# Kernel optimization log

Hardware: AMD Instinct MI355X
Metric: run time of the kernel (lower is better)

The kernel has to match this reference:

```python
import jax, jax.numpy as jnp
import numpy as np

N_USER, N_ITEM = 60000, 60000
N = N_USER + N_ITEM
E_BASE = 1500000
P = 200000
IN_DIM, HID, OUT = 128, 128, 64
K_MAX = 0.5


def setup_inputs() -> dict:
    key = jax.random.key(0)
    ks = jax.random.split(key, 20)
    feat_user = jax.random.normal(ks[0], (N_USER, 256), jnp.float32)
    feat_item = jax.random.normal(ks[1], (N_ITEM, 128), jnp.float32)
    src_b = jax.random.randint(ks[2], (E_BASE,), 0, N, jnp.int32)
    dst_b = jax.random.randint(ks[3], (E_BASE,), 0, N, jnp.int32)
    loops = jnp.arange(N, dtype=jnp.int32)  # dgl.add_self_loop
    src = jnp.concatenate([src_b, loops])
    dst = jnp.concatenate([dst_b, loops])
    pos_src = jax.random.randint(ks[4], (P,), 0, N, jnp.int32)
    pos_dst = jax.random.randint(ks[5], (P,), 0, N, jnp.int32)
    neg_src = jax.random.randint(ks[6], (P,), 0, N, jnp.int32)
    neg_dst = jax.random.randint(ks[7], (P,), 0, N, jnp.int32)
    s = 0.05
    W_user = jax.random.normal(ks[8], (256, IN_DIM), jnp.float32) * s
    b_user = jnp.zeros((IN_DIM,), jnp.float32)
    W_item = jax.random.normal(ks[9], (128, IN_DIM), jnp.float32) * s
    b_item = jnp.zeros((IN_DIM,), jnp.float32)
    W_gat = jax.random.normal(ks[10], (IN_DIM, HID), jnp.float32) * s
    attn_l = jax.random.normal(ks[11], (HID,), jnp.float32) * s
    attn_r = jax.random.normal(ks[12], (HID,), jnp.float32) * s
    gat_bias = jnp.zeros((HID,), jnp.float32)
    W_pred = jax.random.normal(ks[13], (HID, OUT), jnp.float32) * s
    b_pred = jnp.zeros((OUT,), jnp.float32)
    return {
        "feat_user": feat_user, "feat_item": feat_item,
        "W_user": W_user, "b_user": b_user, "W_item": W_item, "b_item": b_item,
        "W_gat": W_gat, "attn_l": attn_l, "attn_r": attn_r, "gat_bias": gat_bias,
        "W_pred": W_pred, "b_pred": b_pred,
        "src": src, "dst": dst,
        "pos_src": pos_src, "pos_dst": pos_dst,
        "neg_src": neg_src, "neg_dst": neg_dst,
        "alpha_T": 1,
    }


def _gat_conv(x, src, dst, W_gat, attn_l, attn_r, gat_bias):
    # DGL GATConv, 1 head: fc (no bias), additive attention, edge softmax over dst.
    z = x @ W_gat                              # [N, HID]
    el = z @ attn_l                            # [N]
    er = z @ attn_r                            # [N]
    e = jax.nn.leaky_relu(el[src] + er[dst], 0.2)   # [E]
    m = jax.ops.segment_max(e, dst, num_segments=N)  # per-dst max (self loops -> no empty segs)
    ex = jnp.exp(e - m[dst])
    ssum = jax.ops.segment_sum(ex, dst, num_segments=N)
    a = ex / ssum[dst]                          # edge softmax coeffs
    msg = z[src] * a[:, None]                   # [E, HID]
    out = jax.ops.segment_sum(msg, dst, num_segments=N) + gat_bias
    return jax.nn.elu(out)                      # activation=F.elu


def _hold_loss(score, k_T):
    l = jax.nn.log_sigmoid(score)
    hold = k_T * jnp.max(l)
    l = jnp.where(l > hold, 0.0, l)
    return -jnp.sum(l)


def reference(feat_user, feat_item, W_user, b_user, W_item, b_item,
              W_gat, attn_l, attn_r, gat_bias, W_pred, b_pred,
              src, dst, pos_src, pos_dst, neg_src, neg_dst, alpha_T):
    # per-type input projection then concat in ntype order (dgl.to_homogeneous)
    hu = feat_user @ W_user + b_user
    hi = feat_item @ W_item + b_item
    x = jnp.concatenate([hu, hi], axis=0)       # [N, IN_DIM]
    h = _gat_conv(x, src, dst, W_gat, attn_l, attn_r, gat_bias)
    pos_score = jnp.sum(h[pos_src] * h[pos_dst], axis=1)
    neg_score = jnp.sum(h[neg_src] * h[neg_dst], axis=1)
    k_T = K_MAX if K_MAX <= alpha_T else alpha_T   # k_T = min(k_max, alpha_T)
    loss = _hold_loss(pos_score, k_T) + _hold_loss(neg_score, k_T)
    out = h[:N_USER] @ W_pred + b_pred          # predict_type 'user' == type id 0
    return loss, out
```

## Files before the change

### kernel.cpp

```cpp
#include <hip/hip_runtime.h>
#include <hip/hip_bf16.h>
#include <math.h>

#define NUSER 60000
#define NITEM 60000
#define NNODE 120000
#define BSH 9
#define NB 235
#define CAP 8192

typedef __attribute__((ext_vector_type(8))) short bf16x8;
typedef __attribute__((ext_vector_type(4))) float f32x4;
typedef __attribute__((ext_vector_type(2))) float f32x2;
typedef __attribute__((ext_vector_type(4))) unsigned short u16x4;

__device__ __forceinline__ float leaky02(float x) { return x > 0.f ? x : 0.2f * x; }

__device__ __forceinline__ float inv_ord(unsigned int u) {
  unsigned int bits = (u & 0x80000000u) ? (u & 0x7FFFFFFFu) : ~u;
  return __uint_as_float(bits);
}
__device__ __forceinline__ unsigned int ord_of(float f) {
  unsigned int u = __float_as_uint(f);
  return (u & 0x80000000u) ? ~u : (u | 0x80000000u);
}
__device__ __forceinline__ short f2bs(float f) {
  __hip_bfloat16 h = __float2bfloat16(f);
  return *reinterpret_cast<short*>(&h);
}

__device__ __forceinline__ void f8fma(f32x2& acc, float w, unsigned int u) {
  f32x2 zz = __builtin_amdgcn_cvt_pk_f32_fp8(u, false);
  f32x2 ww; ww.x = w; ww.y = w;
  acc = __builtin_elementwise_fma(ww, zz, acc);
}
__device__ __forceinline__ void fp8dot(f32x2& acc, unsigned int ua, unsigned int ub) {
  f32x2 a0 = __builtin_amdgcn_cvt_pk_f32_fp8(ua, false);
  f32x2 a1 = __builtin_amdgcn_cvt_pk_f32_fp8(ua, true);
  f32x2 b0 = __builtin_amdgcn_cvt_pk_f32_fp8(ub, false);
  f32x2 b1 = __builtin_amdgcn_cvt_pk_f32_fp8(ub, true);
  acc = __builtin_elementwise_fma(a0, b0, acc);
  acc = __builtin_elementwise_fma(a1, b1, acc);
}

__global__ __launch_bounds__(256) void prep_kernel(
    const float* __restrict__ Wu, const float* __restrict__ bu, const float* __restrict__ Wi,
    const float* __restrict__ bi, const float* __restrict__ Wg, const float* __restrict__ Wp,
    __hip_bfloat16* __restrict__ Bp_u, __hip_bfloat16* __restrict__ Bp_i,
    __hip_bfloat16* __restrict__ Bp_p, float* __restrict__ bf_u, float* __restrict__ bf_i) {
  int t = blockIdx.x * 256 + threadIdx.x;
  if (t < 32768) {
    int j = t & 7, lane = (t >> 3) & 63, rest = t >> 9;
    int nt = rest & 7, ks = rest >> 3;
    int k = ks * 32 + ((lane >> 4) << 3) + j;
    int n = nt * 16 + (lane & 15);
    float acc = 0.f;
#pragma unroll 8
    for (int jj = 0; jj < 128; ++jj) acc = fmaf(Wu[k * 128 + jj], Wg[jj * 128 + n], acc);
    Bp_u[t] = __float2bfloat16(acc);
  } else if (t < 49152) {
    int tt = t - 32768;
    int j = tt & 7, lane = (tt >> 3) & 63, rest = tt >> 9;
    int nt = rest & 7, ks = rest >> 3;
    int k = ks * 32 + ((lane >> 4) << 3) + j;
    int n = nt * 16 + (lane & 15);
    float acc = 0.f;
#pragma unroll 8
    for (int jj = 0; jj < 128; ++jj) acc = fmaf(Wi[k * 128 + jj], Wg[jj * 128 + n], acc);
    Bp_i[tt] = __float2bfloat16(acc);
  } else if (t < 57344) {
    int tt = t - 49152;
    int j = tt & 7, lane = (tt >> 3) & 63, rest = tt >> 9;
    int nt = rest & 3, ks = rest >> 2;
    int k = ks * 32 + ((lane >> 4) << 3) + j;
    int n = nt * 16 + (lane & 15);
    Bp_p[tt] = __float2bfloat16(Wp[k * 64 + n]);
  } else if (t < 57344 + 256) {
    int n = t - 57344;
    if (n < 128) {
      float acc = 0.f;
      for (int jj = 0; jj < 128; ++jj) acc = fmaf(bu[jj], Wg[jj * 128 + n], acc);
      bf_u[n] = acc;
    } else {
      int nn = n - 128;
      float acc = 0.f;
      for (int jj = 0; jj < 128; ++jj) acc = fmaf(bi[jj], Wg[jj * 128 + nn], acc);
      bf_i[nn] = acc;
    }
  }
}

template <int K>
__device__ __forceinline__ void zgemm_body(
    char* smem, const float* __restrict__ A, const __hip_bfloat16* __restrict__ Bp,
    const float* __restrict__ bias, const float* __restrict__ al, const float* __restrict__ ar,
    unsigned char* __restrict__ z8, float* __restrict__ el, float* __restrict__ er, int M,
    int blk) {
  float(*lds)[140] = (float(*)[140])smem;
  const int lane = threadIdx.x & 63, wv = threadIdx.x >> 6;
  const int t = threadIdx.x;
  const int C4 = K / 4;
  for (int f = t; f < 64 * C4; f += 256) {
    int row = f / C4, c4 = f - row * C4;
    int grow = blk * 64 + row;
    if (grow >= M) grow = M - 1;
    float4 a = *(const float4*)(A + (size_t)grow * K + c4 * 4);
    u16x4 pk;
    pk[0] = (unsigned short)f2bs(a.x);
    pk[1] = (unsigned short)f2bs(a.y);
    pk[2] = (unsigned short)f2bs(a.z);
    pk[3] = (unsigned short)f2bs(a.w);
    unsigned int byte = (unsigned int)row * (K * 2) + (unsigned int)c4 * 8;
    byte ^= (row & 7) << 4;
    *(u16x4*)(smem + byte) = pk;
  }
  __syncthreads();
  const bf16x8* bp = (const bf16x8*)Bp;
  const int frow = wv * 16 + (lane & 15);
  f32x4 acc[8] = {};
#pragma unroll
  for (int ks = 0; ks < K / 32; ++ks) {
    unsigned int byte = (unsigned int)frow * (K * 2) + (unsigned int)(ks * 32 + ((lane >> 4) << 3)) * 2;
    byte ^= (frow & 7) << 4;
    bf16x8 af = *(const bf16x8*)(smem + byte);
#pragma unroll
    for (int nt = 0; nt < 8; ++nt) {
      bf16x8 bfr = bp[(ks * 8 + nt) * 64 + lane];
      acc[nt] = __builtin_amdgcn_mfma_f32_16x16x32_bf16(af, bfr, acc[nt], 0, 0, 0);
    }
  }
  __syncthreads();
#pragma unroll
  for (int nt = 0; nt < 8; ++nt) {
    float b = bias[nt * 16 + (lane & 15)];
#pragma unroll
    for (int r = 0; r < 4; ++r)
      lds[wv * 16 + (lane >> 4) * 4 + r][nt * 16 + (lane & 15)] = acc[nt][r] + b;
  }
  __syncthreads();
  int row = threadIdx.x >> 2;
  int q = threadIdx.x & 3;
  int gm = blk * 64 + row;
  float pl = 0.f, pr = 0.f;
  if (gm < M) {
    const float* lrow = &lds[row][q * 32];
#pragma unroll
    for (int v4 = 0; v4 < 4; ++v4) {
      float f[8];
#pragma unroll
      for (int j = 0; j < 8; ++j) {
        f[j] = lrow[v4 * 8 + j];
        int c = q * 32 + v4 * 8 + j;
        pl = fmaf(f[j], al[c], pl);
        pr = fmaf(f[j], ar[c], pr);
      }
      unsigned int w0 = (unsigned int)__builtin_amdgcn_cvt_pk_fp8_f32(f[0], f[1], 0, false);
      w0 = (unsigned int)__builtin_amdgcn_cvt_pk_fp8_f32(f[2], f[3], (int)w0, true);
      unsigned int w1 = (unsigned int)__builtin_amdgcn_cvt_pk_fp8_f32(f[4], f[5], 0, false);
      w1 = (unsigned int)__builtin_amdgcn_cvt_pk_fp8_f32(f[6], f[7], (int)w1, true);
      uint2 st; st.x = w0; st.y = w1;
      *(uint2*)(z8 + (size_t)gm * 128 + q * 32 + v4 * 8) = st;
    }
  }
  pl += __shfl_xor(pl, 1, 64); pl += __shfl_xor(pl, 2, 64);
  pr += __shfl_xor(pr, 1, 64); pr += __shfl_xor(pr, 2, 64);
  if (q == 0 && gm < M) { el[gm] = pl; er[gm] = pr; }
}

__global__ __launch_bounds__(256) void zgemm_kernel(
    const float* __restrict__ Au, const __hip_bfloat16* __restrict__ Bpu,
    const float* __restrict__ bfu, const float* __restrict__ Ai,
    const __hip_bfloat16* __restrict__ Bpi, const float* __restrict__ bfi,
    const float* __restrict__ al, const float* __restrict__ ar, unsigned char* __restrict__ z8,
    float* __restrict__ el, float* __restrict__ er, int GU) {
  __shared__ __align__(16) char smem[64 * 140 * 4];
  if ((int)blockIdx.x < GU)
    zgemm_body<256>(smem, Au, Bpu, bfu, al, ar, z8, el, er, NUSER, blockIdx.x);
  else
    zgemm_body<128>(smem, Ai, Bpi, bfi, al, ar, z8 + (size_t)NUSER * 128, el + NUSER, er + NUSER,
                    NITEM, blockIdx.x - GU);
}

__global__ __launch_bounds__(256) void predgemm_kernel(
    const __hip_bfloat16* __restrict__ h, const __hip_bfloat16* __restrict__ Bp,
    const float* __restrict__ bias, float* __restrict__ out, int M) {
  const int lane = threadIdx.x & 63, wv = threadIdx.x >> 6;
  const int m0 = blockIdx.x * 64 + wv * 16;
  int arow = m0 + (lane & 15);
  if (arow >= M) arow = M - 1;
  const bf16x8* a0 = (const bf16x8*)(h + (size_t)arow * 128) + (lane >> 4);
  const bf16x8* bp = (const bf16x8*)Bp;
  f32x4 acc[4] = {};
#pragma unroll
  for (int ks = 0; ks < 4; ++ks) {
    bf16x8 af = a0[ks * 4];
#pragma unroll
    for (int nt = 0; nt < 4; ++nt) {
      bf16x8 bfr = bp[(ks * 4 + nt) * 64 + lane];
      acc[nt] = __builtin_amdgcn_mfma_f32_16x16x32_bf16(af, bfr, acc[nt], 0, 0, 0);
    }
  }
#pragma unroll
  for (int nt = 0; nt < 4; ++nt) {
    int col = nt * 16 + (lane & 15);
    float b = bias[col];
#pragma unroll
    for (int r = 0; r < 4; ++r) {
      int m = m0 + (lane >> 4) * 4 + r;
      if (m < M) out[(size_t)m * 64 + col] = acc[nt][r] + b;
    }
  }
}

__global__ __launch_bounds__(256) void bcount_kernel(const int* __restrict__ dst,
                                                     int* __restrict__ btotal, int E) {
  __shared__ int cnt[NB];
  for (int t = threadIdx.x; t < NB; t += 256) cnt[t] = 0;
  __syncthreads();
  for (int i = blockIdx.x * 256 + threadIdx.x; i < E; i += gridDim.x * 256)
    atomicAdd(&cnt[dst[i] >> BSH], 1);
  __syncthreads();
  for (int t = threadIdx.x; t < NB; t += 256)
    if (cnt[t]) atomicAdd(&btotal[t], cnt[t]);
}

__global__ void bscan_kernel(const int* __restrict__ btotal, int* __restrict__ bstart,
                             int* __restrict__ gcur) {
  __shared__ int s[256];
  int t = threadIdx.x;
  int v = (t < NB) ? btotal[t] : 0;
  s[t] = v;
  __syncthreads();
  for (int off = 1; off < 256; off <<= 1) {
    int a = (t >= off) ? s[t - off] : 0;
    __syncthreads();
    s[t] += a;
    __syncthreads();
  }
  int excl = s[t] - v;
  if (t < NB) { bstart[t] = excl; gcur[t] = excl; }
  if (t == NB - 1) bstart[NB] = s[t];
}

__global__ __launch_bounds__(256) void bscatter_kernel(const int* __restrict__ src,
                                                       const int* __restrict__ dst,
                                                       int* __restrict__ gcur,
                                                       unsigned int* __restrict__ scratch, int E) {
  __shared__ int cnt[NB];
  __shared__ int base[NB];
  for (int t = threadIdx.x; t < NB; t += 256) cnt[t] = 0;
  __syncthreads();
  const int i0 = blockIdx.x * 4096;
  unsigned int v_[16];
  int b_[16], r_[16];
#pragma unroll
  for (int j = 0; j < 16; ++j) {
    int i = i0 + j * 256 + threadIdx.x;
    b_[j] = -1;
    if (i < E) {
      int d = dst[i];
      int s = src[i];
      int b = d >> BSH;
      b_[j] = b;
      r_[j] = atomicAdd(&cnt[b], 1);
      v_[j] = (unsigned int)s | ((unsigned int)(d & 511) << 17);
    }
  }
  __syncthreads();
  for (int t = threadIdx.x; t < NB; t += 256)
    base[t] = cnt[t] ? atomicAdd(&gcur[t], cnt[t]) : 0;
  __syncthreads();
#pragma unroll
  for (int j = 0; j < 16; ++j)
    if (b_[j] >= 0) scratch[base[b_[j]] + r_[j]] = v_[j];
}

__global__ __launch_bounds__(512) void bsort_kernel(const unsigned int* __restrict__ scratch,
                                                    const int* __restrict__ bstart,
                                                    int* __restrict__ offs, int* __restrict__ ssrc) {
  __shared__ unsigned int buf[CAP];
  __shared__ int cnt[512], scn[512], cur[512];
  int b = blockIdx.x, t = threadIdx.x;
  int s = bstart[b], e = bstart[b + 1], n = e - s;
  int d0 = b << BSH;
  int ndst = NNODE - d0;
  if (ndst > 512) ndst = 512;
  cnt[t] = 0;
  cur[t] = 0;
  __syncthreads();
  bool fit = (n <= CAP);
  if (fit) {
    for (int i = t; i < n; i += 512) {
      unsigned int v = scratch[s + i];
      buf[i] = v;
      atomicAdd(&cnt[v >> 17], 1);
    }
  } else {
    for (int i = t; i < n; i += 512) atomicAdd(&cnt[scratch[s + i] >> 17], 1);
  }
  __syncthreads();
  scn[t] = cnt[t];
  __syncthreads();
  for (int off = 1; off < 512; off <<= 1) {
    int a = (t >= off) ? scn[t - off] : 0;
    __syncthreads();
    scn[t] += a;
    __syncthreads();
  }
  int start = scn[t] - cnt[t];
  if (t < ndst) offs[d0 + t] = s + start;
  if (b == NB - 1 && t == 0) offs[NNODE] = e;
  __syncthreads();
  cnt[t] = start;
  __syncthreads();
  if (fit) {
    for (int i = t; i < n; i += 512) {
      unsigned int v = buf[i];
      int dl = v >> 17;
      int r = atomicAdd(&cur[dl], 1);
      ssrc[s + cnt[dl] + r] = (int)(v & 0x1FFFFu);
    }
  } else {
    for (int i = t; i < n; i += 512) {
      unsigned int v = scratch[s + i];
      int dl = v >> 17;
      int r = atomicAdd(&cur[dl], 1);
      ssrc[s + cnt[dl] + r] = (int)(v & 0x1FFFFu);
    }
  }
}

__global__ __launch_bounds__(256) void aggregate_kernel(
    const unsigned char* __restrict__ z8, const float* __restrict__ el,
    const float* __restrict__ er, const int* __restrict__ offs, const int* __restrict__ ssrc,
    const float* __restrict__ gat_bias, __hip_bfloat16* __restrict__ h,
    unsigned char* __restrict__ h8) {
  __shared__ __align__(16) float2 ew[4][128];
  int wv = threadIdx.x >> 6, lane = threadIdx.x & 63;
  int d = blockIdx.x * 4 + wv;
  int s0 = offs[d], s1 = offs[d + 1];
  int deg = s1 - s0;
  float erd = er[d];
  const unsigned short* zw = (const unsigned short*)z8;
  f32x2 acc = {0.f, 0.f};
  float ssum = 0.f;
  if (deg <= 128) {
    float w0 = 0.f, w1 = 0.f;
    int o0 = 0, o1 = 0;
    if (lane < deg) { int s = ssrc[s0 + lane]; o0 = s << 6; w0 = __expf(leaky02(el[s] + erd)); }
    if (64 + lane < deg) { int s = ssrc[s0 + 64 + lane]; o1 = s << 6; w1 = __expf(leaky02(el[s] + erd)); }
    ew[wv][lane] = make_float2(w0, __int_as_float(o0));
    ew[wv][64 + lane] = make_float2(w1, __int_as_float(o1));
    __builtin_amdgcn_wave_barrier();
    int i = 0;
    for (; i + 8 <= deg; i += 8) {
      float4 p0 = *(const float4*)&ew[wv][i];
      float4 p1 = *(const float4*)&ew[wv][i + 2];
      float4 p2 = *(const float4*)&ew[wv][i + 4];
      float4 p3 = *(const float4*)&ew[wv][i + 6];
      unsigned int u0 = zw[__float_as_uint(p0.y) + lane];
      unsigned int u1 = zw[__float_as_uint(p0.w) + lane];
      unsigned int u2 = zw[__float_as_uint(p1.y) + lane];
      unsigned int u3 = zw[__float_as_uint(p1.w) + lane];
      unsigned int u4 = zw[__float_as_uint(p2.y) + lane];
      unsigned int u5 = zw[__float_as_uint(p2.w) + lane];
      unsigned int u6 = zw[__float_as_uint(p3.y) + lane];
      unsigned int u7 = zw[__float_as_uint(p3.w) + lane];
      ssum += ((p0.x + p0.z) + (p1.x + p1.z)) + ((p2.x + p2.z) + (p3.x + p3.z));
      f8fma(acc, p0.x, u0); f8fma(acc, p0.z, u1);
      f8fma(acc, p1.x, u2); f8fma(acc, p1.z, u3);
      f8fma(acc, p2.x, u4); f8fma(acc, p2.z, u5);
      f8fma(acc, p3.x, u6); f8fma(acc, p3.z, u7);
    }
    for (; i + 2 <= deg; i += 2) {
      float4 p = *(const float4*)&ew[wv][i];
      unsigned int ua = zw[__float_as_uint(p.y) + lane];
      unsigned int ub = zw[__float_as_uint(p.w) + lane];
      ssum += p.x + p.z;
      f8fma(acc, p.x, ua); f8fma(acc, p.z, ub);
    }
    if (i < deg) {
      float2 pp = ew[wv][i];
      unsigned int u = zw[__float_as_uint(pp.y) + lane];
      ssum += pp.x;
      f8fma(acc, pp.x, u);
    }
  } else {
    for (int i2 = s0; i2 < s1; ++i2) {
      int s = ssrc[i2];
      float w = __expf(leaky02(el[s] + erd));
      ssum += w;
      unsigned int u = zw[((unsigned int)s << 6) + lane];
      f8fma(acc, w, u);
    }
  }
  float inv = 1.f / ssum;
  float o0f = acc.x * inv + gat_bias[lane * 2];
  float o1f = acc.y * inv + gat_bias[lane * 2 + 1];
  o0f = (o0f > 0.f) ? o0f : (__expf(o0f) - 1.f);
  o1f = (o1f > 0.f) ? o1f : (__expf(o1f) - 1.f);
  ushort2 ov;
  ov.x = (unsigned short)((unsigned int)f2bs(o0f) & 0xFFFFu);
  ov.y = (unsigned short)((unsigned int)f2bs(o1f) & 0xFFFFu);
  *(ushort2*)((unsigned short*)h + (size_t)d * 128 + lane * 2) = ov;
  int pk8 = __builtin_amdgcn_cvt_pk_fp8_f32(o0f, o1f, 0, false);
  *(unsigned short*)(h8 + (size_t)d * 128 + lane * 2) = (unsigned short)(pk8 & 0xFFFF);
}

__global__ __launch_bounds__(256) void score_kernel(
    const unsigned char* __restrict__ h8, const int* __restrict__ ps, const int* __restrict__ pd,
    const int* __restrict__ ns, const int* __restrict__ nd, float* __restrict__ l_pos,
    float* __restrict__ l_neg, unsigned int* __restrict__ maxacc, int P) {
  const int g16 = threadIdx.x >> 4, l16 = threadIdx.x & 15;
  const uint2* h2 = (const uint2*)h8;
  const int stride = gridDim.x * 16;
  const int tot = 2 * P;
  float mpos = -1e30f, mneg = -1e30f;

  int i = blockIdx.x * 16 + g16;
  int aC = 0, bC = 0;
  if (i < tot) {
    bool n = i >= P; int j = n ? i - P : i;
    aC = n ? ns[j] : ps[j]; bC = n ? nd[j] : pd[j];
  }
  uint2 vaC = {0, 0}, vbC = {0, 0};
  if (i < tot) {
    vaC = h2[(size_t)aC * 16 + l16];
    vbC = h2[(size_t)bC * 16 + l16];
  }
  int i1 = i + stride;
  int aN = 0, bN = 0;
  if (i1 < tot) {
    bool n = i1 >= P; int j = n ? i1 - P : i1;
    aN = n ? ns[j] : ps[j]; bN = n ? nd[j] : pd[j];
  }

  while (i < tot) {
    uint2 vaN = {0, 0}, vbN = {0, 0};
    if (i1 < tot) {
      vaN = h2[(size_t)aN * 16 + l16];
      vbN = h2[(size_t)bN * 16 + l16];
    }
    int i2 = i1 + stride;
    int aN2 = 0, bN2 = 0;
    if (i2 < tot) {
      bool n = i2 >= P; int j = n ? i2 - P : i2;
      aN2 = n ? ns[j] : ps[j]; bN2 = n ? nd[j] : pd[j];
    }
    f32x2 acc = {0.f, 0.f};
    fp8dot(acc, vaC.x, vbC.x);
    fp8dot(acc, vaC.y, vbC.y);
    float s = acc.x + acc.y;
    s += __shfl_xor(s, 1, 16);
    s += __shfl_xor(s, 2, 16);
    s += __shfl_xor(s, 4, 16);
    s += __shfl_xor(s, 8, 16);
    float lv = fminf(s, 0.f) - log1pf(__expf(-fabsf(s)));
    bool neg = i >= P;
    int j = neg ? i - P : i;
    if (l16 == 0) (neg ? l_neg : l_pos)[j] = lv;
    if (neg) mneg = fmaxf(mneg, lv); else mpos = fmaxf(mpos, lv);
    i = i1; i1 = i2;
    aC = aN; bC = bN; aN = aN2; bN = bN2;
    vaC = vaN; vbC = vbN;
  }
  __shared__ float red0[256], red1[256];
  red0[threadIdx.x] = mpos;
  red1[threadIdx.x] = mneg;
  __syncthreads();
  for (int off = 128; off; off >>= 1) {
    if (threadIdx.x < off) {
      red0[threadIdx.x] = fmaxf(red0[threadIdx.x], red0[threadIdx.x + off]);
      red1[threadIdx.x] = fmaxf(red1[threadIdx.x], red1[threadIdx.x + off]);
    }
    __syncthreads();
  }
  if (threadIdx.x == 0) {
    atomicMax(maxacc + 0, ord_of(red0[0]));
    atomicMax(maxacc + 1, ord_of(red1[0]));
  }
}

__global__ __launch_bounds__(256) void loss_sum_kernel(const float* __restrict__ l_pos,
                                                       const float* __restrict__ l_neg,
                                                       const unsigned int* __restrict__ maxacc,
                                                       const int* __restrict__ alpha,
                                                       float* __restrict__ sums, int P) {
  __shared__ float sdata[256];
  int which = blockIdx.x >> 9;
  const float* l = which ? l_neg : l_pos;
  float a = (float)alpha[0];
  float kT = (0.5f <= a) ? 0.5f : a;
  float hold = kT * inv_ord(maxacc[which]);
  float s = 0.f;
  for (int i = (blockIdx.x & 511) * 256 + threadIdx.x; i < P; i += 512 * 256) {
    float v = l[i];
    if (!(v > hold)) s += v;
  }
  sdata[threadIdx.x] = s;
  __syncthreads();
  for (int off = 128; off; off >>= 1) {
    if (threadIdx.x < off) sdata[threadIdx.x] += sdata[threadIdx.x + off];
    __syncthreads();
  }
  if (threadIdx.x == 0) atomicAdd(&sums[which], sdata[0]);
}

__global__ void final_kernel(const float* __restrict__ sums, float* __restrict__ out) {
  out[0] = -(sums[0] + sums[1]);
}

extern "C" void kernel_launch(void* const* d_in, const int* in_sizes, int n_in,
                              void* d_out, int out_size, void* d_ws, size_t ws_size,
                              hipStream_t stream) {
  const float* feat_user = (const float*)d_in[0];
  const float* feat_item = (const float*)d_in[1];
  const float* W_user = (const float*)d_in[2];
  const float* b_user = (const float*)d_in[3];
  const float* W_item = (const float*)d_in[4];
  const float* b_item = (const float*)d_in[5];
  const float* W_gat = (const float*)d_in[6];
  const float* attn_l = (const float*)d_in[7];
  const float* attn_r = (const float*)d_in[8];
  const float* gat_bias = (const float*)d_in[9];
  const float* W_pred = (const float*)d_in[10];
  const float* b_pred = (const float*)d_in[11];
  const int* src = (const int*)d_in[12];
  const int* dst = (const int*)d_in[13];
  const int* pos_src = (const int*)d_in[14];
  const int* pos_dst = (const int*)d_in[15];
  const int* neg_src = (const int*)d_in[16];
  const int* neg_dst = (const int*)d_in[17];
  const int* alpha = (const int*)d_in[18];
  const int E = in_sizes[12];
  const int P = in_sizes[14];

  char* p = (char*)d_ws;
  auto alloc = [&](size_t bytes) {
    char* r = p;
    p += (bytes + 255) & ~(size_t)255;
    return r;
  };
  unsigned char* z8 = (unsigned char*)alloc((size_t)NNODE * 128);
  __hip_bfloat16* h = (__hip_bfloat16*)alloc((size_t)NNODE * 128 * 2);
  unsigned char* h8 = (unsigned char*)alloc((size_t)NNODE * 128);
  float* el = (float*)alloc((size_t)NNODE * 4);
  float* er = (float*)alloc((size_t)NNODE * 4);
  __hip_bfloat16* Bp_u = (__hip_bfloat16*)alloc(256 * 128 * 2);
  __hip_bfloat16* Bp_i = (__hip_bfloat16*)alloc(128 * 128 * 2);
  __hip_bfloat16* Bp_p = (__hip_bfloat16*)alloc(128 * 64 * 2);
  float* bf_u = (float*)alloc(128 * 4);
  float* bf_i = (float*)alloc(128 * 4);
  int* offs = (int*)alloc((size_t)(NNODE + 4) * 4);
  int* ssrc = (int*)alloc((size_t)E * 4);
  unsigned int* scratch = (unsigned int*)alloc((size_t)E * 4);
  float* l_pos = (float*)alloc((size_t)P * 4);
  float* l_neg = (float*)alloc((size_t)P * 4);
  int* bstart = (int*)alloc((NB + 1) * 4);
  int* gcur = (int*)alloc(NB * 4);
  int* btotal = (int*)alloc((NB + 8) * 4);
  unsigned int* maxacc = (unsigned int*)(btotal + NB);
  float* sums = (float*)(maxacc + 2);

  float* out_loss = (float*)d_out;
  float* out_pred = out_loss + 1;

  hipMemsetAsync(btotal, 0, (NB + 8) * 4, stream);

  prep_kernel<<<225, 256, 0, stream>>>(W_user, b_user, W_item, b_item, W_gat, W_pred, Bp_u, Bp_i,
                                       Bp_p, bf_u, bf_i);

  bcount_kernel<<<512, 256, 0, stream>>>(dst, btotal, E);
  bscan_kernel<<<1, 256, 0, stream>>>(btotal, bstart, gcur);
  bscatter_kernel<<<(E + 4095) / 4096, 256, 0, stream>>>(src, dst, gcur, scratch, E);
  bsort_kernel<<<NB, 512, 0, stream>>>(scratch, bstart, offs, ssrc);

  const int GU = (NUSER + 63) / 64, GI = (NITEM + 63) / 64;
  zgemm_kernel<<<GU + GI, 256, 0, stream>>>(feat_user, Bp_u, bf_u, feat_item, Bp_i, bf_i, attn_l,
                                            attn_r, z8, el, er, GU);

  aggregate_kernel<<<NNODE / 4, 256, 0, stream>>>(z8, el, er, offs, ssrc, gat_bias, h, h8);

  score_kernel<<<2048, 256, 0, stream>>>(h8, pos_src, pos_dst, neg_src, neg_dst, l_pos, l_neg,
                                         maxacc, P);
  loss_sum_kernel<<<1024, 256, 0, stream>>>(l_pos, l_neg, maxacc, alpha, sums, P);
  final_kernel<<<1, 1, 0, stream>>>(sums, out_loss);

  predgemm_kernel<<<(NUSER + 63) / 64, 256, 0, stream>>>(h, Bp_p, b_pred, out_pred, NUSER);

  (void)n_in; (void)out_size; (void)ws_size;
}
```

Measured before the change: 258.1 us.

## Fuse independent kernels via block-range dispatch and batch score gathers

Merges the weight-prep and bucket-count kernels into one launch, and the edge scatter with the z-GEMM, by splitting the grid into block ranges so independent work runs together. The final loss write is folded into the prediction GEMM, which removes one launch. The score kernel now handles four pairs per group with the gathers issued together instead of software prefetching, and its grid grows to 6250 blocks. This cuts launch count and lets independent stages overlap, but the scatter blocks now share a launch with the heavier GEMM blocks and so carry that kernel's LDS allocation.

```diff
diff --git a/kernel.cpp b/kernel.cpp
--- a/kernel.cpp
+++ b/kernel.cpp
@@ -43,12 +43,25 @@
   acc = __builtin_elementwise_fma(a1, b1, acc);
 }
 
-__global__ __launch_bounds__(256) void prep_kernel(
+__global__ __launch_bounds__(256) void prep_count_kernel(
     const float* __restrict__ Wu, const float* __restrict__ bu, const float* __restrict__ Wi,
     const float* __restrict__ bi, const float* __restrict__ Wg, const float* __restrict__ Wp,
     __hip_bfloat16* __restrict__ Bp_u, __hip_bfloat16* __restrict__ Bp_i,
-    __hip_bfloat16* __restrict__ Bp_p, float* __restrict__ bf_u, float* __restrict__ bf_i) {
-  int t = blockIdx.x * 256 + threadIdx.x;
+    __hip_bfloat16* __restrict__ Bp_p, float* __restrict__ bf_u, float* __restrict__ bf_i,
+    const int* __restrict__ dst, int* __restrict__ btotal, int E) {
+  __shared__ int cnt[NB];
+  if (blockIdx.x < 512) {
+    int bid = blockIdx.x;
+    for (int t = threadIdx.x; t < NB; t += 256) cnt[t] = 0;
+    __syncthreads();
+    for (int i = bid * 256 + threadIdx.x; i < E; i += 512 * 256)
+      atomicAdd(&cnt[dst[i] >> BSH], 1);
+    __syncthreads();
+    for (int t = threadIdx.x; t < NB; t += 256)
+      if (cnt[t]) atomicAdd(&btotal[t], cnt[t]);
+    return;
+  }
+  int t = (blockIdx.x - 512) * 256 + threadIdx.x;
   if (t < 32768) {
     int j = t & 7, lane = (t >> 3) & 63, rest = t >> 9;
     int nt = rest & 7, ks = rest >> 3;
@@ -90,6 +103,24 @@
   }
 }
 
+__global__ void bscan_kernel(const int* __restrict__ btotal, int* __restrict__ bstart,
+                             int* __restrict__ gcur) {
+  __shared__ int s[256];
+  int t = threadIdx.x;
+  int v = (t < NB) ? btotal[t] : 0;
+  s[t] = v;
+  __syncthreads();
+  for (int off = 1; off < 256; off <<= 1) {
+    int a = (t >= off) ? s[t - off] : 0;
+    __syncthreads();
+    s[t] += a;
+    __syncthreads();
+  }
+  int excl = s[t] - v;
+  if (t < NB) { bstart[t] = excl; gcur[t] = excl; }
+  if (t == NB - 1) bstart[NB] = s[t];
+}
+
 template <int K>
 __device__ __forceinline__ void zgemm_body(
     char* smem, const float* __restrict__ A, const __hip_bfloat16* __restrict__ Bp,
@@ -167,112 +198,52 @@
   if (q == 0 && gm < M) { el[gm] = pl; er[gm] = pr; }
 }
 
-__global__ __launch_bounds__(256) void zgemm_kernel(
+__global__ __launch_bounds__(256) void zgemm_scatter_kernel(
     const float* __restrict__ Au, const __hip_bfloat16* __restrict__ Bpu,
     const float* __restrict__ bfu, const float* __restrict__ Ai,
     const __hip_bfloat16* __restrict__ Bpi, const float* __restrict__ bfi,
     const float* __restrict__ al, const float* __restrict__ ar, unsigned char* __restrict__ z8,
-    float* __restrict__ el, float* __restrict__ er, int GU) {
+    float* __restrict__ el, float* __restrict__ er, int SC, int GU,
+    const int* __restrict__ src, const int* __restrict__ dst, int* __restrict__ gcur,
+    unsigned int* __restrict__ scratch, int E) {
   __shared__ __align__(16) char smem[64 * 140 * 4];
-  if ((int)blockIdx.x < GU)
-    zgemm_body<256>(smem, Au, Bpu, bfu, al, ar, z8, el, er, NUSER, blockIdx.x);
+  int bx = blockIdx.x;
+  if (bx < SC) {
+    int* cnt = (int*)smem;
+    int* basep = cnt + NB;
+    for (int t = threadIdx.x; t < NB; t += 256) cnt[t] = 0;
+    __syncthreads();
+    const int i0 = bx * 4096;
+    unsigned int v_[16];
+    int b_[16], r_[16];
+#pragma unroll
+    for (int j = 0; j < 16; ++j) {
+      int i = i0 + j * 256 + threadIdx.x;
+      b_[j] = -1;
+      if (i < E) {
+        int d = dst[i];
+        int s = src[i];
+        int b = d >> BSH;
+        b_[j] = b;
+        r_[j] = atomicAdd(&cnt[b], 1);
+        v_[j] = (unsigned int)s | ((unsigned int)(d & 511) << 17);
+      }
+    }
+    __syncthreads();
+    for (int t = threadIdx.x; t < NB; t += 256)
+      basep[t] = cnt[t] ? atomicAdd(&gcur[t], cnt[t]) : 0;
+    __syncthreads();
+#pragma unroll
+    for (int j = 0; j < 16; ++j)
+      if (b_[j] >= 0) scratch[basep[b_[j]] + r_[j]] = v_[j];
+    return;
+  }
+  int gb = bx - SC;
+  if (gb < GU)
+    zgemm_body<256>(smem, Au, Bpu, bfu, al, ar, z8, el, er, NUSER, gb);
   else
     zgemm_body<128>(smem, Ai, Bpi, bfi, al, ar, z8 + (size_t)NUSER * 128, el + NUSER, er + NUSER,
-                    NITEM, blockIdx.x - GU);
-}
-
-__global__ __launch_bounds__(256) void predgemm_kernel(
-    const __hip_bfloat16* __restrict__ h, const __hip_bfloat16* __restrict__ Bp,
-    const float* __restrict__ bias, float* __restrict__ out, int M) {
-  const int lane = threadIdx.x & 63, wv = threadIdx.x >> 6;
-  const int m0 = blockIdx.x * 64 + wv * 16;
-  int arow = m0 + (lane & 15);
-  if (arow >= M) arow = M - 1;
-  const bf16x8* a0 = (const bf16x8*)(h + (size_t)arow * 128) + (lane >> 4);
-  const bf16x8* bp = (const bf16x8*)Bp;
-  f32x4 acc[4] = {};
-#pragma unroll
-  for (int ks = 0; ks < 4; ++ks) {
-    bf16x8 af = a0[ks * 4];
-#pragma unroll
-    for (int nt = 0; nt < 4; ++nt) {
-      bf16x8 bfr = bp[(ks * 4 + nt) * 64 + lane];
-      acc[nt] = __builtin_amdgcn_mfma_f32_16x16x32_bf16(af, bfr, acc[nt], 0, 0, 0);
-    }
-  }
-#pragma unroll
-  for (int nt = 0; nt < 4; ++nt) {
-    int col = nt * 16 + (lane & 15);
-    float b = bias[col];
-#pragma unroll
-    for (int r = 0; r < 4; ++r) {
-      int m = m0 + (lane >> 4) * 4 + r;
-      if (m < M) out[(size_t)m * 64 + col] = acc[nt][r] + b;
-    }
-  }
-}
-
-__global__ __launch_bounds__(256) void bcount_kernel(const int* __restrict__ dst,
-                                                     int* __restrict__ btotal, int E) {
-  __shared__ int cnt[NB];
-  for (int t = threadIdx.x; t < NB; t += 256) cnt[t] = 0;
-  __syncthreads();
-  for (int i = blockIdx.x * 256 + threadIdx.x; i < E; i += gridDim.x * 256)
-    atomicAdd(&cnt[dst[i] >> BSH], 1);
-  __syncthreads();
-  for (int t = threadIdx.x; t < NB; t += 256)
-    if (cnt[t]) atomicAdd(&btotal[t], cnt[t]);
-}
-
-__global__ void bscan_kernel(const int* __restrict__ btotal, int* __restrict__ bstart,
-                             int* __restrict__ gcur) {
-  __shared__ int s[256];
-  int t = threadIdx.x;
-  int v = (t < NB) ? btotal[t] : 0;
-  s[t] = v;
-  __syncthreads();
-  for (int off = 1; off < 256; off <<= 1) {
-    int a = (t >= off) ? s[t - off] : 0;
-    __syncthreads();
-    s[t] += a;
-    __syncthreads();
-  }
-  int excl = s[t] - v;
-  if (t < NB) { bstart[t] = excl; gcur[t] = excl; }
-  if (t == NB - 1) bstart[NB] = s[t];
-}
-
-__global__ __launch_bounds__(256) void bscatter_kernel(const int* __restrict__ src,
-                                                       const int* __restrict__ dst,
-                                                       int* __restrict__ gcur,
-                                                       unsigned int* __restrict__ scratch, int E) {
-  __shared__ int cnt[NB];
-  __shared__ int base[NB];
-  for (int t = threadIdx.x; t < NB; t += 256) cnt[t] = 0;
-  __syncthreads();
-  const int i0 = blockIdx.x * 4096;
-  unsigned int v_[16];
-  int b_[16], r_[16];
-#pragma unroll
-  for (int j = 0; j < 16; ++j) {
-    int i = i0 + j * 256 + threadIdx.x;
-    b_[j] = -1;
-    if (i < E) {
-      int d = dst[i];
-      int s = src[i];
-      int b = d >> BSH;
-      b_[j] = b;
-      r_[j] = atomicAdd(&cnt[b], 1);
-      v_[j] = (unsigned int)s | ((unsigned int)(d & 511) << 17);
-    }
-  }
-  __syncthreads();
-  for (int t = threadIdx.x; t < NB; t += 256)
-    base[t] = cnt[t] ? atomicAdd(&gcur[t], cnt[t]) : 0;
-  __syncthreads();
-#pragma unroll
-  for (int j = 0; j < 16; ++j)
-    if (b_[j] >= 0) scratch[base[b_[j]] + r_[j]] = v_[j];
+                    NITEM, gb - GU);
 }
 
 __global__ __launch_bounds__(512) void bsort_kernel(const unsigned int* __restrict__ scratch,
@@ -413,56 +384,47 @@
     float* __restrict__ l_neg, unsigned int* __restrict__ maxacc, int P) {
   const int g16 = threadIdx.x >> 4, l16 = threadIdx.x & 15;
   const uint2* h2 = (const uint2*)h8;
-  const int stride = gridDim.x * 16;
+  const int ngroups = gridDim.x * 16;
   const int tot = 2 * P;
   float mpos = -1e30f, mneg = -1e30f;
-
-  int i = blockIdx.x * 16 + g16;
-  int aC = 0, bC = 0;
-  if (i < tot) {
-    bool n = i >= P; int j = n ? i - P : i;
-    aC = n ? ns[j] : ps[j]; bC = n ? nd[j] : pd[j];
-  }
-  uint2 vaC = {0, 0}, vbC = {0, 0};
-  if (i < tot) {
-    vaC = h2[(size_t)aC * 16 + l16];
-    vbC = h2[(size_t)bC * 16 + l16];
-  }
-  int i1 = i + stride;
-  int aN = 0, bN = 0;
-  if (i1 < tot) {
-    bool n = i1 >= P; int j = n ? i1 - P : i1;
-    aN = n ? ns[j] : ps[j]; bN = n ? nd[j] : pd[j];
-  }
-
-  while (i < tot) {
-    uint2 vaN = {0, 0}, vbN = {0, 0};
-    if (i1 < tot) {
-      vaN = h2[(size_t)aN * 16 + l16];
-      vbN = h2[(size_t)bN * 16 + l16];
-    }
-    int i2 = i1 + stride;
-    int aN2 = 0, bN2 = 0;
-    if (i2 < tot) {
-      bool n = i2 >= P; int j = n ? i2 - P : i2;
-      aN2 = n ? ns[j] : ps[j]; bN2 = n ? nd[j] : pd[j];
-    }
-    f32x2 acc = {0.f, 0.f};
-    fp8dot(acc, vaC.x, vbC.x);
-    fp8dot(acc, vaC.y, vbC.y);
-    float s = acc.x + acc.y;
-    s += __shfl_xor(s, 1, 16);
-    s += __shfl_xor(s, 2, 16);
-    s += __shfl_xor(s, 4, 16);
-    s += __shfl_xor(s, 8, 16);
-    float lv = fminf(s, 0.f) - log1pf(__expf(-fabsf(s)));
-    bool neg = i >= P;
-    int j = neg ? i - P : i;
-    if (l16 == 0) (neg ? l_neg : l_pos)[j] = lv;
-    if (neg) mneg = fmaxf(mneg, lv); else mpos = fmaxf(mpos, lv);
-    i = i1; i1 = i2;
-    aC = aN; bC = bN; aN = aN2; bN = bN2;
-    vaC = vaN; vbC = vbN;
+  const int gid = blockIdx.x * 16 + g16;
+  for (int base = gid * 4; base < tot; base += ngroups * 4) {
+    int a_[4], b_[4];
+#pragma unroll
+    for (int k = 0; k < 4; ++k) {
+      int i = base + k;
+      if (i < tot) {
+        bool n = i >= P;
+        int j = n ? i - P : i;
+        a_[k] = n ? ns[j] : ps[j];
+        b_[k] = n ? nd[j] : pd[j];
+      } else { a_[k] = 0; b_[k] = 0; }
+    }
+    uint2 va_[4], vb_[4];
+#pragma unroll
+    for (int k = 0; k < 4; ++k) {
+      va_[k] = h2[(size_t)a_[k] * 16 + l16];
+      vb_[k] = h2[(size_t)b_[k] * 16 + l16];
+    }
+#pragma unroll
+    for (int k = 0; k < 4; ++k) {
+      int i = base + k;
+      if (i < tot) {
+        f32x2 acc = {0.f, 0.f};
+        fp8dot(acc, va_[k].x, vb_[k].x);
+        fp8dot(acc, va_[k].y, vb_[k].y);
+        float s = acc.x + acc.y;
+        s += __shfl_xor(s, 1, 16);
+        s += __shfl_xor(s, 2, 16);
+        s += __shfl_xor(s, 4, 16);
+        s += __shfl_xor(s, 8, 16);
+        float lv = fminf(s, 0.f) - log1pf(__expf(-fabsf(s)));
+        bool neg = i >= P;
+        int j = neg ? i - P : i;
+        if (l16 == 0) (neg ? l_neg : l_pos)[j] = lv;
+        if (neg) mneg = fmaxf(mneg, lv); else mpos = fmaxf(mpos, lv);
+      }
+    }
   }
   __shared__ float red0[256], red1[256];
   red0[threadIdx.x] = mpos;
@@ -506,8 +468,38 @@
   if (threadIdx.x == 0) atomicAdd(&sums[which], sdata[0]);
 }
 
-__global__ void final_kernel(const float* __restrict__ sums, float* __restrict__ out) {
-  out[0] = -(sums[0] + sums[1]);
+__global__ __launch_bounds__(256) void predgemm_kernel(
+    const __hip_bfloat16* __restrict__ h, const __hip_bfloat16* __restrict__ Bp,
+    const float* __restrict__ bias, const float* __restrict__ sums, float* __restrict__ out,
+    int M) {
+  if (blockIdx.x == 0 && threadIdx.x == 0) out[0] = -(sums[0] + sums[1]);
+  float* outp = out + 1;
+  const int lane = threadIdx.x & 63, wv = threadIdx.x >> 6;
+  const int m0 = blockIdx.x * 64 + wv * 16;
+  int arow = m0 + (lane & 15);
+  if (arow >= M) arow = M - 1;
+  const bf16x8* a0 = (const bf16x8*)(h + (size_t)arow * 128) + (lane >> 4);
+  const bf16x8* bp = (const bf16x8*)Bp;
+  f32x4 acc[4] = {};
+#pragma unroll
+  for (int ks = 0; ks < 4; ++ks) {
+    bf16x8 af = a0[ks * 4];
+#pragma unroll
+    for (int nt = 0; nt < 4; ++nt) {
+      bf16x8 bfr = bp[(ks * 4 + nt) * 64 + lane];
+      acc[nt] = __builtin_amdgcn_mfma_f32_16x16x32_bf16(af, bfr, acc[nt], 0, 0, 0);
+    }
+  }
+#pragma unroll
+  for (int nt = 0; nt < 4; ++nt) {
+    int col = nt * 16 + (lane & 15);
+    float b = bias[col];
+#pragma unroll
+    for (int r = 0; r < 4; ++r) {
+      int m = m0 + (lane >> 4) * 4 + r;
+      if (m < M) outp[(size_t)m * 64 + col] = acc[nt][r] + b;
+    }
+  }
 }
 
 extern "C" void kernel_launch(void* const* d_in, const int* in_sizes, int n_in,
@@ -562,31 +554,23 @@
   unsigned int* maxacc = (unsigned int*)(btotal + NB);
   float* sums = (float*)(maxacc + 2);
 
-  float* out_loss = (float*)d_out;
-  float* out_pred = out_loss + 1;
-
   hipMemsetAsync(btotal, 0, (NB + 8) * 4, stream);
 
-  prep_kernel<<<225, 256, 0, stream>>>(W_user, b_user, W_item, b_item, W_gat, W_pred, Bp_u, Bp_i,
-                                       Bp_p, bf_u, bf_i);
-
-  bcount_kernel<<<512, 256, 0, stream>>>(dst, btotal, E);
+  prep_count_kernel<<<512 + 225, 256, 0, stream>>>(W_user, b_user, W_item, b_item, W_gat, W_pred,
+                                                   Bp_u, Bp_i, Bp_p, bf_u, bf_i, dst, btotal, E);
   bscan_kernel<<<1, 256, 0, stream>>>(btotal, bstart, gcur);
-  bscatter_kernel<<<(E + 4095) / 4096, 256, 0, stream>>>(src, dst, gcur, scratch, E);
+  const int GU = (NUSER + 63) / 64, GI = (NITEM + 63) / 64;
+  const int SC = (E + 4095) / 4096;
+  zgemm_scatter_kernel<<<SC + GU + GI, 256, 0, stream>>>(feat_user, Bp_u, bf_u, feat_item, Bp_i,
+                                                         bf_i, attn_l, attn_r, z8, el, er, SC, GU,
+                                                         src, dst, gcur, scratch, E);
   bsort_kernel<<<NB, 512, 0, stream>>>(scratch, bstart, offs, ssrc);
-
-  const int GU = (NUSER + 63) / 64, GI = (NITEM + 63) / 64;
-  zgemm_kernel<<<GU + GI, 256, 0, stream>>>(feat_user, Bp_u, bf_u, feat_item, Bp_i, bf_i, attn_l,
-                                            attn_r, z8, el, er, GU);
-
   aggregate_kernel<<<NNODE / 4, 256, 0, stream>>>(z8, el, er, offs, ssrc, gat_bias, h, h8);
-
-  score_kernel<<<2048, 256, 0, stream>>>(h8, pos_src, pos_dst, neg_src, neg_dst, l_pos, l_neg,
+  score_kernel<<<6250, 256, 0, stream>>>(h8, pos_src, pos_dst, neg_src, neg_dst, l_pos, l_neg,
                                          maxacc, P);
   loss_sum_kernel<<<1024, 256, 0, stream>>>(l_pos, l_neg, maxacc, alpha, sums, P);
-  final_kernel<<<1, 1, 0, stream>>>(sums, out_loss);
-
-  predgemm_kernel<<<(NUSER + 63) / 64, 256, 0, stream>>>(h, Bp_p, b_pred, out_pred, NUSER);
+  predgemm_kernel<<<(NUSER + 63) / 64, 256, 0, stream>>>(h, Bp_p, b_pred, sums, (float*)d_out,
+                                                         NUSER);
 
   (void)n_in; (void)out_size; (void)ws_size;
 }
```

Result: slower. 325.2 us (+26.0%).
